# Kernel tuning notes

Hardware: AMD Instinct MI355X
Metric: run time of the kernel (lower is better)

Reference implementation:

```python
import jax, jax.numpy as jnp
import numpy as np

B, N, IN_DIM, EMB, HEADS, M, ITERS = 8, 4096, 1024, 512, 4, 256, 6
DH = EMB // HEADS
SCALE = DH ** -0.5
RES_K = 33  # residual depthwise conv kernel size (TransMIL / nystrom-attention default)


def setup_inputs() -> dict:
    key = jax.random.key(0)
    ks = iter(jax.random.split(key, 40))
    def rn(shape, s=0.02):
        return jax.random.normal(next(ks), shape, jnp.float32) * s
    inp = {"X": jax.random.normal(next(ks), (B, N, IN_DIM), jnp.float32)}
    inp["few_w"] = rn((IN_DIM, EMB)); inp["few_b"] = jnp.zeros((EMB,), jnp.float32)
    inp["cls_token"] = rn((1, 1, EMB), 1.0)
    for i in (1, 2):
        inp[f"l{i}_ln_g"] = jnp.ones((EMB,), jnp.float32)
        inp[f"l{i}_ln_b"] = jnp.zeros((EMB,), jnp.float32)
        inp[f"l{i}_qkv_w"] = rn((EMB, 3 * EMB))
        inp[f"l{i}_out_w"] = rn((EMB, EMB))
        inp[f"l{i}_out_b"] = jnp.zeros((EMB,), jnp.float32)
        inp[f"l{i}_res_k"] = rn((HEADS, 1, RES_K, 1))
    for ksz in (7, 5, 3):
        inp[f"ppeg_k{ksz}"] = rn((EMB, 1, ksz, ksz))
        inp[f"ppeg_b{ksz}"] = jnp.zeros((EMB,), jnp.float32)
    inp["norm_g"] = jnp.ones((EMB,), jnp.float32)
    inp["norm_b"] = jnp.zeros((EMB,), jnp.float32)
    inp["cls_w"] = rn((EMB, 1)); inp["cls_b"] = jnp.zeros((1,), jnp.float32)
    return inp


def _ln(x, g, b):
    mu = x.mean(-1, keepdims=True)
    var = x.var(-1, keepdims=True)
    return (x - mu) / jnp.sqrt(var + 1e-5) * g + b


def _pinv(x, iters):
    # Moore-Penrose iterative pseudo-inverse of (..., m, m)
    abs_x = jnp.abs(x)
    z = jnp.swapaxes(x, -1, -2) / (abs_x.sum(-1).max() * abs_x.sum(-2).max())
    I = jnp.eye(x.shape[-1], dtype=x.dtype)
    for _ in range(iters):
        xz = x @ z
        z = 0.25 * z @ (13 * I - xz @ (15 * I - xz @ (7 * I - xz)))
    return z


def _nystrom_layer(x, ln_g, ln_b, qkv_w, out_w, out_b, res_k):
    # pre-norm transformer layer with Nystrom attention + residual depthwise conv
    b, n, d = x.shape
    h = _ln(x, ln_g, ln_b)
    pad = (-n) % M  # left-pad so seq divisible by n_landmarks
    hp = jnp.pad(h, ((0, 0), (pad, 0), (0, 0)))
    n_p = n + pad
    q, k, v = jnp.split(hp @ qkv_w, 3, axis=-1)
    def to_heads(t):
        return t.reshape(b, n_p, HEADS, DH).transpose(0, 2, 1, 3)  # (b,h,n,dh)
    q, k, v = to_heads(q) * SCALE, to_heads(k), to_heads(v)
    l = n_p // M
    q_l = q.reshape(b, HEADS, M, l, DH).mean(3)  # landmark means
    k_l = k.reshape(b, HEADS, M, l, DH).mean(3)
    a1 = jax.nn.softmax(jnp.einsum('bhid,bhjd->bhij', q, k_l), -1)    # (b,h,n,m)
    a2 = jax.nn.softmax(jnp.einsum('bhid,bhjd->bhij', q_l, k_l), -1)  # (b,h,m,m)
    a3 = jax.nn.softmax(jnp.einsum('bhid,bhjd->bhij', q_l, k), -1)    # (b,h,m,n)
    out = a1 @ (_pinv(a2, ITERS) @ (a3 @ v))
    # residual depthwise conv over sequence, one channel per head
    res = jax.lax.conv_general_dilated(
        v, res_k, (1, 1), ((RES_K // 2, RES_K // 2), (0, 0)),
        dimension_numbers=('NCHW', 'OIHW', 'NCHW'), feature_group_count=HEADS)
    out = out + res
    out = out.transpose(0, 2, 1, 3).reshape(b, n_p, d) @ out_w + out_b
    return x + out[:, -n:]


def _dwconv(x, k, bias, pad):
    y = jax.lax.conv_general_dilated(
        x, k, (1, 1), ((pad, pad), (pad, pad)),
        dimension_numbers=('NCHW', 'OIHW', 'NCHW'), feature_group_count=EMB)
    return y + bias[None, :, None, None]


def _ppeg(x, H, W, k7, b7, k5, b5, k3, b3):
    b, _, c = x.shape
    cls_t, feat = x[:, :1], x[:, 1:]
    f = feat.transpose(0, 2, 1).reshape(b, c, H, W)
    y = f + _dwconv(f, k7, b7, 3) + _dwconv(f, k5, b5, 2) + _dwconv(f, k3, b3, 1)
    y = y.reshape(b, c, H * W).transpose(0, 2, 1)
    return jnp.concatenate([cls_t, y], axis=1)


def _forward(X, few_w, few_b, cls_token,
             l1_ln_g, l1_ln_b, l1_qkv_w, l1_out_w, l1_out_b, l1_res_k,
             l2_ln_g, l2_ln_b, l2_qkv_w, l2_out_w, l2_out_b, l2_res_k,
             ppeg_k7, ppeg_b7, ppeg_k5, ppeg_b5, ppeg_k3, ppeg_b3,
             norm_g, norm_b, cls_w, cls_b):
    b, bag = X.shape[0], X.shape[1]
    h = X @ few_w + few_b
    ps = int(np.ceil(np.sqrt(bag)))
    add = ps * ps - bag
    h = jnp.concatenate([h, h[:, :add]], axis=1)  # pad bag to perfect square
    h = jnp.concatenate([jnp.broadcast_to(cls_token, (b, 1, EMB)), h], axis=1)
    h = _nystrom_layer(h, l1_ln_g, l1_ln_b, l1_qkv_w, l1_out_w, l1_out_b, l1_res_k)
    h = _ppeg(h, ps, ps, ppeg_k7, ppeg_b7, ppeg_k5, ppeg_b5, ppeg_k3, ppeg_b3)
    h = _nystrom_layer(h, l2_ln_g, l2_ln_b, l2_qkv_w, l2_out_w, l2_out_b, l2_res_k)
    h = _ln(h, norm_g, norm_b)
    return (h[:, 0] @ cls_w + cls_b).squeeze(-1)  # (batch,) bag logits


def reference(X, few_w, few_b, cls_token,
              l1_ln_g, l1_ln_b, l1_qkv_w, l1_out_w, l1_out_b, l1_res_k,
              l2_ln_g, l2_ln_b, l2_qkv_w, l2_out_w, l2_out_b, l2_res_k,
              ppeg_k7, ppeg_b7, ppeg_k5, ppeg_b5, ppeg_k3, ppeg_b3,
              norm_g, norm_b, cls_w, cls_b):
    return _forward(X, few_w, few_b, cls_token,
                    l1_ln_g, l1_ln_b, l1_qkv_w, l1_out_w, l1_out_b, l1_res_k,
                    l2_ln_g, l2_ln_b, l2_qkv_w, l2_out_w, l2_out_b, l2_res_k,
                    ppeg_k7, ppeg_b7, ppeg_k5, ppeg_b5, ppeg_k3, ppeg_b3,
                    norm_g, norm_b, cls_w, cls_b)
```

## Files before the change

### kernel.cpp

```cpp
#include <hip/hip_runtime.h>

constexpr int BATCH = 8;
constexpr int NTOK  = 4097;
constexpr int NP    = 4352;
constexpr int PADR  = 255;
constexpr int EMBD  = 512;
constexpr int DHD   = 128;
constexpr int LSUB  = 17;
constexpr float SCALE_F = 0.08838834764831845f;

constexpr int PPS   = 72;
constexpr int PPLN  = 72 * 70;
constexpr long long TPAD_FLOATS = (long long)BATCH * EMBD * PPLN;

typedef unsigned short u16;
typedef short   s16x8 __attribute__((ext_vector_type(8)));
typedef u16     u16x4 __attribute__((ext_vector_type(4)));
typedef float   f32x4 __attribute__((ext_vector_type(4)));

__device__ __forceinline__ u16 f2bf(float x) {
    unsigned u = __float_as_uint(x);
    u += 0x7fffu + ((u >> 16) & 1u);
    return (u16)(u >> 16);
}
__device__ __forceinline__ float bf2f(u16 h) {
    return __uint_as_float(((unsigned)h) << 16);
}

__device__ __forceinline__ float block_sum256(float v) {
    __shared__ float tmp[4];
    __syncthreads();
#pragma unroll
    for (int off = 32; off > 0; off >>= 1) v += __shfl_down(v, off, 64);
    int t = threadIdx.x;
    if ((t & 63) == 0) tmp[t >> 6] = v;
    __syncthreads();
    return tmp[0] + tmp[1] + tmp[2] + tmp[3];
}

__device__ __forceinline__ float block_max256(float v) {
    __shared__ float tmp[4];
    __syncthreads();
#pragma unroll
    for (int off = 32; off > 0; off >>= 1) v = fmaxf(v, __shfl_down(v, off, 64));
    int t = threadIdx.x;
    if ((t & 63) == 0) tmp[t >> 6] = v;
    __syncthreads();
    return fmaxf(fmaxf(tmp[0], tmp[1]), fmaxf(tmp[2], tmp[3]));
}

struct GemmP {
    const float* A; const float* B; float* C; const float* bias;
    long long As1, As2, Bs1, Bs2, Cs1, Cs2;
    int Adiv, Bdiv, Cdiv;
    int Am, Bk, Bn, Cm, Arow, Crow;
    int M, N, K, nb;
    float alpha; int accum;
    float bdiagc; int btrans; float cdiagc; int ctrans;
};

constexpr int LDSTR = 40;
constexpr int AH = 0, AL = 2560, BHs = 5120, BLs = 7680;

__global__ __launch_bounds__(256) void gemm_k(GemmP p) {
    __shared__ u16 lds[10240];
    const int bz = blockIdx.z;
    const float* Ab = p.A + (long long)(bz / p.Adiv) * p.As1 + (long long)(bz % p.Adiv) * p.As2;
    const float* Bb = p.B + (long long)(bz / p.Bdiv) * p.Bs1 + (long long)(bz % p.Bdiv) * p.Bs2;
    float*       Cb = p.C + (long long)(bz / p.Cdiv) * p.Cs1 + (long long)(bz % p.Cdiv) * p.Cs2;
    const int m0 = blockIdx.y * 64, n0 = blockIdx.x * 64;
    const int t = threadIdx.x;
    const int wave = t >> 6, lane = t & 63;
    const int wm = (wave & 1) * 32, wn = (wave >> 1) * 32;
    const int quad = lane >> 4, l15 = lane & 15;

    f32x4 acc[2][2];
#pragma unroll
    for (int i = 0; i < 2; ++i)
#pragma unroll
        for (int j = 0; j < 2; ++j) acc[i][j] = (f32x4){0.f, 0.f, 0.f, 0.f};

    for (int k0 = 0; k0 < p.K; k0 += 32) {
        {
            const int ar = t >> 2, ac = (t & 3) * 8;
            float v[8];
            if (m0 + ar < p.M) {
                const float* s = Ab + (long long)(m0 + ar + p.Arow) * p.Am + (k0 + ac);
                float4 x0 = *(const float4*)s, x1 = *(const float4*)(s + 4);
                v[0] = x0.x; v[1] = x0.y; v[2] = x0.z; v[3] = x0.w;
                v[4] = x1.x; v[5] = x1.y; v[6] = x1.z; v[7] = x1.w;
            } else {
#pragma unroll
                for (int i = 0; i < 8; ++i) v[i] = 0.f;
            }
            u16 h[8], l[8];
#pragma unroll
            for (int i = 0; i < 8; ++i) { h[i] = f2bf(v[i]); l[i] = f2bf(v[i] - bf2f(h[i])); }
            const int off = ar * LDSTR + ac;
            u16x4 a0, a1, b0, b1;
#pragma unroll
            for (int i = 0; i < 4; ++i) { a0[i] = h[i]; a1[i] = h[i + 4]; b0[i] = l[i]; b1[i] = l[i + 4]; }
            *(u16x4*)&lds[AH + off] = a0; *(u16x4*)&lds[AH + off + 4] = a1;
            *(u16x4*)&lds[AL + off] = b0; *(u16x4*)&lds[AL + off + 4] = b1;
        }
        if (p.Bn == 1) {
            const int bk = t >> 3, n8 = (t & 7) * 8;
            const float* s = Bb + (long long)(k0 + bk) * p.Bk + (n0 + n8);
            float4 x0 = *(const float4*)s, x1 = *(const float4*)(s + 4);
            float v[8] = {x0.x, x0.y, x0.z, x0.w, x1.x, x1.y, x1.z, x1.w};
            if (p.btrans) {
                const int gk = k0 + bk;
#pragma unroll
                for (int i = 0; i < 8; ++i)
                    v[i] = (gk == n0 + n8 + i ? p.bdiagc : 0.f) - v[i];
            }
#pragma unroll
            for (int i = 0; i < 8; ++i) {
                int j = (i + (t & 7)) & 7;
                u16 h = f2bf(v[j]);
                lds[BHs + (n8 + j) * LDSTR + bk] = h;
                lds[BLs + (n8 + j) * LDSTR + bk] = f2bf(v[j] - bf2f(h));
            }
        } else {
            const int bn = t >> 2, k8 = (t & 3) * 8;
            const float* s = Bb + (long long)(n0 + bn) * p.Bn + (k0 + k8);
            float4 x0 = *(const float4*)s, x1 = *(const float4*)(s + 4);
            float v[8] = {x0.x, x0.y, x0.z, x0.w, x1.x, x1.y, x1.z, x1.w};
            u16 h[8], l[8];
#pragma unroll
            for (int i = 0; i < 8; ++i) { h[i] = f2bf(v[i]); l[i] = f2bf(v[i] - bf2f(h[i])); }
            const int off = bn * LDSTR + k8;
            u16x4 a0, a1, b0, b1;
#pragma unroll
            for (int i = 0; i < 4; ++i) { a0[i] = h[i]; a1[i] = h[i + 4]; b0[i] = l[i]; b1[i] = l[i + 4]; }
            *(u16x4*)&lds[BHs + off] = a0; *(u16x4*)&lds[BHs + off + 4] = a1;
            *(u16x4*)&lds[BLs + off] = b0; *(u16x4*)&lds[BLs + off + 4] = b1;
        }
        __syncthreads();

        s16x8 ah[2], al[2], bh[2], bl[2];
#pragma unroll
        for (int mi = 0; mi < 2; ++mi) {
            const int off = (wm + mi * 16 + l15) * LDSTR + quad * 8;
            u16x4 q0 = *(const u16x4*)&lds[AH + off], q1 = *(const u16x4*)&lds[AH + off + 4];
            u16x4 r0 = *(const u16x4*)&lds[AL + off], r1 = *(const u16x4*)&lds[AL + off + 4];
            s16x8 fh, fl;
#pragma unroll
            for (int i = 0; i < 4; ++i) { fh[i] = q0[i]; fh[i + 4] = q1[i]; fl[i] = r0[i]; fl[i + 4] = r1[i]; }
            ah[mi] = fh; al[mi] = fl;
        }
#pragma unroll
        for (int ni = 0; ni < 2; ++ni) {
            const int off = (wn + ni * 16 + l15) * LDSTR + quad * 8;
            u16x4 q0 = *(const u16x4*)&lds[BHs + off], q1 = *(const u16x4*)&lds[BHs + off + 4];
            u16x4 r0 = *(const u16x4*)&lds[BLs + off], r1 = *(const u16x4*)&lds[BLs + off + 4];
            s16x8 fh, fl;
#pragma unroll
            for (int i = 0; i < 4; ++i) { fh[i] = q0[i]; fh[i + 4] = q1[i]; fl[i] = r0[i]; fl[i + 4] = r1[i]; }
            bh[ni] = fh; bl[ni] = fl;
        }
#pragma unroll
        for (int mi = 0; mi < 2; ++mi)
#pragma unroll
            for (int ni = 0; ni < 2; ++ni) {
                acc[mi][ni] = __builtin_amdgcn_mfma_f32_16x16x32_bf16(ah[mi], bh[ni], acc[mi][ni], 0, 0, 0);
                acc[mi][ni] = __builtin_amdgcn_mfma_f32_16x16x32_bf16(ah[mi], bl[ni], acc[mi][ni], 0, 0, 0);
                acc[mi][ni] = __builtin_amdgcn_mfma_f32_16x16x32_bf16(al[mi], bh[ni], acc[mi][ni], 0, 0, 0);
            }
        __syncthreads();
    }

#pragma unroll
    for (int mi = 0; mi < 2; ++mi)
#pragma unroll
        for (int ni = 0; ni < 2; ++ni) {
            const int n = n0 + wn + ni * 16 + l15;
#pragma unroll
            for (int r = 0; r < 4; ++r) {
                const int m = m0 + wm + mi * 16 + quad * 4 + r;
                if (m >= p.M) continue;
                float v = p.alpha * acc[mi][ni][r];
                if (p.bias) v += p.bias[n];
                if (p.ctrans) v = (m == n ? p.cdiagc : 0.f) - v;
                float* dst = Cb + (long long)(m + p.Crow) * p.Cm + n;
                if (p.accum) *dst += v; else *dst = v;
            }
        }
}

__global__ void cls_set_k(float* H0, const float* cls) {
    int t = blockIdx.x * 256 + threadIdx.x;
    int b = t >> 9, c = t & 511;
    H0[(long long)b * NTOK * EMBD + c] = cls[c];
}

__global__ __launch_bounds__(256) void ln_pad_k(const float* __restrict__ H0,
                                                float* __restrict__ out,
                                                const float* g, const float* bb) {
    int row = blockIdx.x, b = blockIdx.y, t = threadIdx.x;
    float* o = out + ((long long)b * NP + row) * EMBD;
    if (row < PADR) { o[t] = 0.f; o[t + 256] = 0.f; return; }
    const float* x = H0 + ((long long)b * NTOK + (row - PADR)) * EMBD;
    float v0 = x[t], v1 = x[t + 256];
    float mu = block_sum256(v0 + v1) * (1.f / EMBD);
    float d0 = v0 - mu, d1 = v1 - mu;
    float var = block_sum256(d0 * d0 + d1 * d1) * (1.f / EMBD);
    float rs = 1.f / sqrtf(var + 1e-5f);
    o[t]       = d0 * rs * g[t]       + bb[t];
    o[t + 256] = d1 * rs * g[t + 256] + bb[t + 256];
}

__global__ void landmark_k(const float* __restrict__ QKV, float* __restrict__ QL,
                           float* __restrict__ KL) {
    long long idx = (long long)blockIdx.x * 256 + threadIdx.x;
    int d = idx & 127; int i = (int)((idx >> 7) & 255); int bh = (int)(idx >> 15);
    int b = bh >> 2, h = bh & 3;
    const float* base = QKV + (long long)b * NP * 1536 + (long long)i * LSUB * 1536 + h * DHD + d;
    float sq = 0.f, sk = 0.f;
#pragma unroll
    for (int j = 0; j < LSUB; ++j) { sq += base[j * 1536]; sk += base[j * 1536 + EMBD]; }
    QL[idx] = sq * (1.f / LSUB);
    KL[idx] = sk * (1.f / LSUB);
}

__global__ __launch_bounds__(256) void softmax256_k(float* __restrict__ X) {
    long long row = (long long)blockIdx.x * 4 + (threadIdx.x >> 6);
    int lane = threadIdx.x & 63;
    float4* p = (float4*)(X + row * 256) + lane;
    float4 v = *p;
    float m = fmaxf(fmaxf(v.x, v.y), fmaxf(v.z, v.w));
#pragma unroll
    for (int off = 32; off > 0; off >>= 1) m = fmaxf(m, __shfl_xor(m, off, 64));
    float ex = __expf(v.x - m), ey = __expf(v.y - m), ez = __expf(v.z - m), ew = __expf(v.w - m);
    float s = ex + ey + ez + ew;
#pragma unroll
    for (int off = 32; off > 0; off >>= 1) s += __shfl_xor(s, off, 64);
    float inv = 1.f / s;
    *p = make_float4(ex * inv, ey * inv, ez * inv, ew * inv);
}

__global__ __launch_bounds__(256) void softmax_k(float* __restrict__ X, int L) {
    float4* p = (float4*)(X + (long long)blockIdx.x * L);
    int nv = L >> 2, t = threadIdx.x;
    float m = -1e30f;
    for (int i = t; i < nv; i += 256) {
        float4 v = p[i];
        m = fmaxf(m, fmaxf(fmaxf(v.x, v.y), fmaxf(v.z, v.w)));
    }
    m = block_max256(m);
    float s = 0.f;
    for (int i = t; i < nv; i += 256) {
        float4 v = p[i];
        v.x = __expf(v.x - m); v.y = __expf(v.y - m); v.z = __expf(v.z - m); v.w = __expf(v.w - m);
        p[i] = v;
        s += v.x + v.y + v.z + v.w;
    }
    s = block_sum256(s);
    float inv = 1.f / s;
    for (int i = t; i < nv; i += 256) {
        float4 v = p[i];
        p[i] = make_float4(v.x * inv, v.y * inv, v.z * inv, v.w * inv);
    }
}

__global__ __launch_bounds__(256) void pinv_absmax_k(const float* __restrict__ X, float* red) {
    int bh = blockIdx.x, t = threadIdx.x;
    const float* x = X + (long long)bh * 65536;
    float rs = 0.f, cs = 0.f;
    for (int j = 0; j < 256; ++j) { rs += fabsf(x[t * 256 + j]); cs += fabsf(x[j * 256 + t]); }
    float mr = block_max256(rs);
    float mc = block_max256(cs);
    if (t == 0) { red[bh] = mr; red[32 + bh] = mc; }
}

__global__ void pinv_scalar_k(const float* red, float* inv) {
    float mr = 0.f, mc = 0.f;
    for (int i = 0; i < 32; ++i) { mr = fmaxf(mr, red[i]); mc = fmaxf(mc, red[32 + i]); }
    inv[0] = 1.f / (mr * mc);
}

__global__ void pinv_tinit_k(const float* __restrict__ X, const float* __restrict__ inv,
                             float* __restrict__ Z) {
    long long idx = (long long)blockIdx.x * 256 + threadIdx.x;
    int j = (int)(idx & 255); int i = (int)((idx >> 8) & 255); long long bh = idx >> 16;
    Z[idx] = X[(bh << 16) + ((long long)j << 8) + i] * inv[0];
}

__global__ void resconv_k(const float* __restrict__ QKV, const float* __restrict__ rk,
                          float* __restrict__ ATT2) {
    long long idx = (long long)blockIdx.x * 256 + threadIdx.x;
    if (idx >= (long long)BATCH * NTOK * EMBD) return;
    int c = (int)(idx & 511); long long r = idx >> 9;
    int n = PADR + (int)(r % NTOK); int b = (int)(r / NTOK);
    int h = c >> 7, d = c & 127;
    const float* vb = QKV + (long long)b * NP * 1536 + 1024 + h * DHD + d;
    float acc = 0.f;
#pragma unroll
    for (int u = 0; u < 33; ++u) {
        int nn = n + u - 16;
        if (nn >= 0 && nn < NP) acc += vb[(long long)nn * 1536] * rk[h * 33 + u];
    }
    ATT2[((long long)b * NP + n) * EMBD + c] += acc;
}

__global__ void wsum_k(const float* __restrict__ k7, const float* __restrict__ k5,
                       const float* __restrict__ k3, const float* __restrict__ b7,
                       const float* __restrict__ b5, const float* __restrict__ b3,
                       float* __restrict__ W) {
    int idx = blockIdx.x * 256 + threadIdx.x;
    if (idx < 25088) {
        int c = idx / 49, i = idx - c * 49;
        int dy = i / 7, dx = i - dy * 7;
        float w = k7[idx];
        if (dy >= 1 && dy <= 5 && dx >= 1 && dx <= 5) w += k5[c * 25 + (dy - 1) * 5 + (dx - 1)];
        if (dy >= 2 && dy <= 4 && dx >= 2 && dx <= 4) w += k3[c * 9 + (dy - 2) * 3 + (dx - 2)];
        W[idx] = w;
    } else if (idx < 25600) {
        int c = idx - 25088;
        W[25088 + c] = b7[c] + b5[c] + b3[c];
    }
}

__global__ __launch_bounds__(256) void tin_k(const float* __restrict__ H0,
                                             float* __restrict__ Tpad) {
    __shared__ float lds[64][65];
    const int y = blockIdx.x, c0 = blockIdx.y * 64, b = blockIdx.z;
    const int t = threadIdx.x;
    const int pc = t & 63, pr4 = t >> 6;
    const float* src = H0 + ((long long)b * NTOK + 1 + y * 64) * EMBD + c0;
#pragma unroll
    for (int i = 0; i < 16; ++i) {
        int pr = pr4 + i * 4;
        lds[pr][pc] = src[(long long)pr * EMBD + pc];
    }
    __syncthreads();
    const int xw = t & 63, cw4 = t >> 6;
#pragma unroll
    for (int i = 0; i < 16; ++i) {
        int cw = cw4 + i * 4;
        Tpad[(long long)(b * 512 + c0 + cw) * PPLN + (3 + y) * PPS + 3 + xw] = lds[xw][cw];
    }
}

__global__ __launch_bounds__(256, 4) void conv7_k(const float* __restrict__ Tpad,
                                                  const float* __restrict__ Wall,
                                                  float* __restrict__ Tout) {
    const int bc = blockIdx.x;
    const int c = bc & 511;
    const int t = threadIdx.x;
    const int x = t & 63, band = t >> 6;
    const int y0 = band * 16;
    const float* in = Tpad + (long long)bc * PPLN + x;
    float* outp = Tout + (long long)bc * 4096 + x;

    float W[49];
#pragma unroll
    for (int i = 0; i < 49; ++i) W[i] = Wall[c * 49 + i];
    const float bias = Wall[25088 + c];

    float win[7][7];
#pragma unroll
    for (int j = 0; j < 6; ++j)
#pragma unroll
        for (int d = 0; d < 7; ++d)
            win[j][d] = in[(y0 + j) * PPS + d];

#pragma unroll
    for (int yy = 0; yy < 16; ++yy) {
        const int slot = (6 + yy) % 7;
#pragma unroll
        for (int d = 0; d < 7; ++d)
            win[slot][d] = in[(y0 + yy + 6) * PPS + d];
        float s = bias + win[(yy + 3) % 7][3];
#pragma unroll
        for (int dy = 0; dy < 7; ++dy) {
            const int r = (yy + dy) % 7;
#pragma unroll
            for (int dx = 0; dx < 7; ++dx)
                s += W[dy * 7 + dx] * win[r][dx];
        }
        outp[(y0 + yy) * 64] = s;
    }
}

__global__ __launch_bounds__(256) void tout_k(const float* __restrict__ Tout,
                                              float* __restrict__ H0) {
    __shared__ float lds[64][65];
    const int y = blockIdx.x, c0 = blockIdx.y * 64, b = blockIdx.z;
    const int t = threadIdx.x;
    const int xl = t & 63, cl4 = t >> 6;
#pragma unroll
    for (int i = 0; i < 16; ++i) {
        int cl = cl4 + i * 4;
        lds[xl][cl] = Tout[(long long)(b * 512 + c0 + cl) * 4096 + y * 64 + xl];
    }
    __syncthreads();
    const int pc = t & 63, pl4 = t >> 6;
    float* dst = H0 + ((long long)b * NTOK + 1 + y * 64) * EMBD + c0;
#pragma unroll
    for (int i = 0; i < 16; ++i) {
        int pl = pl4 + i * 4;
        dst[(long long)pl * EMBD + pc] = lds[pl][pc];
    }
}

__global__ __launch_bounds__(256) void head_k(const float* __restrict__ H0, const float* g,
                                              const float* bb, const float* cw, const float* cb,
                                              float* __restrict__ out) {
    int b = blockIdx.x, t = threadIdx.x;
    const float* x = H0 + (long long)b * NTOK * EMBD;
    float v0 = x[t], v1 = x[t + 256];
    float mu = block_sum256(v0 + v1) * (1.f / EMBD);
    float d0 = v0 - mu, d1 = v1 - mu;
    float var = block_sum256(d0 * d0 + d1 * d1) * (1.f / EMBD);
    float rs = 1.f / sqrtf(var + 1e-5f);
    float y0 = d0 * rs * g[t] + bb[t];
    float y1 = d1 * rs * g[t + 256] + bb[t + 256];
    float s = block_sum256(y0 * cw[t] + y1 * cw[t + 256]);
    if (t == 0) out[b] = s + cb[0];
}

extern "C" void kernel_launch(void* const* d_in, const int* in_sizes, int n_in,
                              void* d_out, int out_size, void* d_ws, size_t ws_size,
                              hipStream_t stream) {
    (void)in_sizes; (void)n_in; (void)out_size; (void)ws_size;
    const float* X        = (const float*)d_in[0];
    const float* few_w    = (const float*)d_in[1];
    const float* few_b    = (const float*)d_in[2];
    const float* cls_tok  = (const float*)d_in[3];
    const float* ln_g[2]  = {(const float*)d_in[4],  (const float*)d_in[10]};
    const float* ln_b[2]  = {(const float*)d_in[5],  (const float*)d_in[11]};
    const float* qkv_w[2] = {(const float*)d_in[6],  (const float*)d_in[12]};
    const float* out_w[2] = {(const float*)d_in[7],  (const float*)d_in[13]};
    const float* out_b[2] = {(const float*)d_in[8],  (const float*)d_in[14]};
    const float* res_k[2] = {(const float*)d_in[9],  (const float*)d_in[15]};
    const float* k7 = (const float*)d_in[16]; const float* b7 = (const float*)d_in[17];
    const float* k5 = (const float*)d_in[18]; const float* b5 = (const float*)d_in[19];
    const float* k3 = (const float*)d_in[20]; const float* b3 = (const float*)d_in[21];
    const float* norm_g = (const float*)d_in[22]; const float* norm_b = (const float*)d_in[23];
    const float* cls_w  = (const float*)d_in[24]; const float* cls_b  = (const float*)d_in[25];
    float* out = (float*)d_out;

    float* ws  = (float*)d_ws;
    float* H0  = ws;
    float* LNH = H0  + 16781312LL;
    float* QKV = LNH + 17825792LL;
    float* A3  = QKV + 53477376LL;
    float* QL  = A3  + 35651584LL;
    float* KL  = QL  + 1048576LL;
    float* A2  = KL  + 1048576LL;
    float* KV  = A2  + 2097152LL;
    float* ZKV = KV  + 1048576LL;
    float* RED = ZKV + 1048576LL;
    float* Zb0 = A3;
    float* Zb1 = A3 + 2097152LL;
    float* XZm = A3 + 4194304LL;
    float* Tpad = QKV;
    float* Tout = QKV + TPAD_FLOATS;
    float* WSUM = A3;

    auto gemmx = [&](const float* A, long long As1, long long As2, int Adiv, int Am, int Arow,
                     const float* Bm, long long Bs1, long long Bs2, int Bdiv, int Bk, int Bn,
                     float* C, long long Cs1, long long Cs2, int Cdiv, int Cm, int Crow,
                     int M, int N, int K, int nb, float alpha, int accum, const float* bias,
                     float bdiagc, int btrans, float cdiagc, int ctrans) {
        GemmP p;
        p.A = A; p.B = Bm; p.C = C; p.bias = bias;
        p.As1 = As1; p.As2 = As2; p.Bs1 = Bs1; p.Bs2 = Bs2; p.Cs1 = Cs1; p.Cs2 = Cs2;
        p.Adiv = Adiv; p.Bdiv = Bdiv; p.Cdiv = Cdiv;
        p.Am = Am; p.Bk = Bk; p.Bn = Bn; p.Cm = Cm; p.Arow = Arow; p.Crow = Crow;
        p.M = M; p.N = N; p.K = K; p.nb = nb; p.alpha = alpha; p.accum = accum;
        p.bdiagc = bdiagc; p.btrans = btrans; p.cdiagc = cdiagc; p.ctrans = ctrans;
        dim3 grid(N / 64, (M + 63) / 64, nb);
        gemm_k<<<grid, 256, 0, stream>>>(p);
    };
    auto gemm = [&](const float* A, long long As1, long long As2, int Adiv, int Am, int Arow,
                    const float* Bm, long long Bs1, long long Bs2, int Bdiv, int Bk, int Bn,
                    float* C, long long Cs1, long long Cs2, int Cdiv, int Cm, int Crow,
                    int M, int N, int K, int nb, float alpha, int accum, const float* bias) {
        gemmx(A, As1, As2, Adiv, Am, Arow, Bm, Bs1, Bs2, Bdiv, Bk, Bn,
              C, Cs1, Cs2, Cdiv, Cm, Crow, M, N, K, nb, alpha, accum, bias, 0.f, 0, 0.f, 0);
    };

    cls_set_k<<<16, 256, 0, stream>>>(H0, cls_tok);
    gemm(X, 4194304LL, 0, 1, 1024, 0,
         few_w, 0, 0, 1, 512, 1,
         H0, 2097664LL, 0, 1, 512, 1,
         4096, 512, 1024, BATCH, 1.f, 0, few_b);

    for (int L = 0; L < 2; ++L) {
        ln_pad_k<<<dim3(NP, BATCH), 256, 0, stream>>>(H0, LNH, ln_g[L], ln_b[L]);
        gemm(LNH, 0, 0, 1, 512, 0,
             qkv_w[L], 0, 0, 1, 1536, 1,
             QKV, 0, 0, 1, 1536, 0,
             BATCH * NP, 1536, 512, 1, 1.f, 0, nullptr);
        landmark_k<<<4096, 256, 0, stream>>>(QKV, QL, KL);
        gemm(QL, 32768LL, 0, 1, 128, 0,
             KL, 32768LL, 0, 1, 1, 128,
             A2, 65536LL, 0, 1, 256, 0,
             256, 256, 128, 32, SCALE_F, 0, nullptr);
        softmax256_k<<<2048, 256, 0, stream>>>(A2);
        gemm(QL, 32768LL, 0, 1, 128, 0,
             QKV + 512, 6680064LL, 128LL, 4, 1, 1536,
             A3, 1114112LL, 0, 1, 4352, 0,
             256, 4352, 128, 32, SCALE_F, 0, nullptr);
        softmax_k<<<8192, 256, 0, stream>>>(A3, 4352);
        gemm(A3, 1114112LL, 0, 1, 4352, 0,
             QKV + 1024, 6680064LL, 128LL, 4, 1536, 1,
             KV, 32768LL, 0, 1, 128, 0,
             256, 128, 4352, 32, 1.f, 0, nullptr);
        pinv_absmax_k<<<32, 256, 0, stream>>>(A2, RED);
        pinv_scalar_k<<<1, 1, 0, stream>>>(RED, RED + 64);
        pinv_tinit_k<<<8192, 256, 0, stream>>>(A2, RED + 64, Zb0);
        float* zc = Zb0; float* zn = Zb1;
        for (int it = 0; it < 6; ++it) {
            float* U1 = A3 + 6291456LL;
            float* U2 = A3 + 8388608LL;
            gemm(A2, 65536LL, 0, 1, 256, 0, zc, 65536LL, 0, 1, 256, 1,
                 XZm, 65536LL, 0, 1, 256, 0, 256, 256, 256, 32, 1.f, 0, nullptr);
            gemmx(XZm, 65536LL, 0, 1, 256, 0, XZm, 65536LL, 0, 1, 256, 1,
                  U1, 65536LL, 0, 1, 256, 0, 256, 256, 256, 32, 1.f, 0, nullptr,
                  7.f, 1, 15.f, 1);
            gemmx(XZm, 65536LL, 0, 1, 256, 0, U1, 65536LL, 0, 1, 256, 1,
                  U2, 65536LL, 0, 1, 256, 0, 256, 256, 256, 32, 1.f, 0, nullptr,
                  0.f, 0, 13.f, 1);
            gemm(zc, 65536LL, 0, 1, 256, 0, U2, 65536LL, 0, 1, 256, 1,
                 zn, 65536LL, 0, 1, 256, 0, 256, 256, 256, 32, 0.25f, 0, nullptr);
            float* t2 = zc; zc = zn; zn = t2;
        }
        gemm(zc, 65536LL, 0, 1, 256, 0,
             KV, 32768LL, 0, 1, 128, 1,
             ZKV, 32768LL, 0, 1, 128, 0,
             256, 128, 256, 32, 1.f, 0, nullptr);
        gemm(QKV, 6680064LL, 128LL, 4, 1536, 0,
             KL, 32768LL, 0, 1, 1, 128,
             A3, 1114112LL, 0, 1, 256, 0,
             4352, 256, 128, 32, SCALE_F, 0, nullptr);
        softmax256_k<<<34816, 256, 0, stream>>>(A3);
        gemm(A3, 1114112LL, 0, 1, 256, 0,
             ZKV, 32768LL, 0, 1, 128, 1,
             LNH, 2228224LL, 128LL, 4, 512, 0,
             4352, 128, 256, 32, 1.f, 0, nullptr);
        resconv_k<<<65552, 256, 0, stream>>>(QKV, res_k[L], LNH);
        gemm(LNH, 2228224LL, 0, 1, 512, PADR,
             out_w[L], 0, 0, 1, 512, 1,
             H0, 2097664LL, 0, 1, 512, 0,
             NTOK, 512, 512, BATCH, 1.f, 1, out_b[L]);

        if (L == 0) {
            hipMemsetAsync(Tpad, 0, TPAD_FLOATS * sizeof(float), stream);
            wsum_k<<<101, 256, 0, stream>>>(k7, k5, k3, b7, b5, b3, WSUM);
            tin_k<<<dim3(64, 8, 8), 256, 0, stream>>>(H0, Tpad);
            conv7_k<<<4096, 256, 0, stream>>>(Tpad, WSUM, Tout);
            tout_k<<<dim3(64, 8, 8), 256, 0, stream>>>(Tout, H0);
        }
    }

    head_k<<<BATCH, 256, 0, stream>>>(H0, norm_g, norm_b, cls_w, cls_b, out);
}
```

Measured before the change: 4.561 ms.

## Add split-bf16 3-pass MFMA GEMM for large projections and attention scores

Adds a new GEMM kernel using a larger 128x256 tile that multiplies split bf16 hi/lo pairs with three MFMA passes (hi*hi, hi*lo, lo*hi) to approximate fp32 accuracy. It is used for the feature, QKV and output projections and for the two big landmark score GEMMs. Operands are pre-split by new split/transpose kernels, and LayerNorm now writes hi/lo bf16 directly. The kernel-3 softmax GEMM is moved earlier and workspace buffers are re-aliased. The extra split passes and memory traffic are the cost, and the three-pass bf16 scheme may lose a little accuracy.

```diff
diff --git a/kernel.cpp b/kernel.cpp
--- a/kernel.cpp
+++ b/kernel.cpp
@@ -188,6 +188,141 @@
         }
 }
 
+struct SplitP {
+    const float* src; u16* dh; u16* dl;
+    long long s1, s2, rstride, dstride, total;
+    int div, R, C8;
+    float scale;
+};
+__global__ __launch_bounds__(256) void split_k(SplitP p) {
+    long long idx = (long long)blockIdx.x * 256 + threadIdx.x;
+    if (idx >= p.total) return;
+    int c8 = (int)(idx % p.C8);
+    long long tmp = idx / p.C8;
+    int r  = (int)(tmp % p.R);
+    int bz = (int)(tmp / p.R);
+    const float* s = p.src + (long long)(bz / p.div) * p.s1 + (long long)(bz % p.div) * p.s2
+                   + (long long)r * p.rstride + c8 * 8;
+    float4 x0 = *(const float4*)s, x1 = *(const float4*)(s + 4);
+    float v[8] = {x0.x, x0.y, x0.z, x0.w, x1.x, x1.y, x1.z, x1.w};
+    s16x8 hv, lv;
+#pragma unroll
+    for (int i = 0; i < 8; ++i) {
+        float sv = v[i] * p.scale;
+        u16 h = f2bf(sv);
+        hv[i] = (short)h;
+        lv[i] = (short)f2bf(sv - bf2f(h));
+    }
+    long long doff = (long long)bz * p.dstride + (long long)r * (p.C8 * 8) + c8 * 8;
+    *(s16x8*)&p.dh[doff] = hv;
+    *(s16x8*)&p.dl[doff] = lv;
+}
+
+__global__ __launch_bounds__(256) void splitT_k(const float* __restrict__ src,
+                                                u16* __restrict__ dh, u16* __restrict__ dl,
+                                                int K, int N) {
+    int idx = blockIdx.x * 256 + threadIdx.x;
+    if (idx >= N * K) return;
+    int n = idx / K, k = idx - n * K;
+    float v = src[(long long)k * N + n];
+    u16 h = f2bf(v);
+    dh[idx] = h;
+    dl[idx] = f2bf(v - bf2f(h));
+}
+
+struct GemmBtP {
+    const u16 *Ah, *Al, *Bh, *Bl;
+    float* C; const float* bias;
+    long long Abs, Bbs, Cbs;
+    int M, N, K, Cm, Crow, accum;
+};
+
+__global__ __launch_bounds__(256, 2) void gemm_bt_k(GemmBtP p) {
+    __shared__ u16 lds[10240];
+    const int bz = blockIdx.z;
+    const u16* Ahb = p.Ah + (long long)bz * p.Abs;
+    const u16* Alb = p.Al + (long long)bz * p.Abs;
+    const u16* Bhb = p.Bh + (long long)bz * p.Bbs;
+    const u16* Blb = p.Bl + (long long)bz * p.Bbs;
+    float*     Cb  = p.C  + (long long)bz * p.Cbs;
+    const int m0 = blockIdx.y * 128, n0 = blockIdx.x * 256;
+    const int t = threadIdx.x;
+    const int wave = t >> 6, lane = t & 63;
+    const int wm = (wave & 1) * 64, wn = (wave >> 1) * 128;
+    const int quad = lane >> 4, l15 = lane & 15;
+    const int K = p.K;
+
+    const int r0 = t >> 2, c0 = (t & 3) * 8;
+    const int ga0 = (m0 + r0      < p.M) ? (m0 + r0)      : (p.M - 1);
+    const int ga1 = (m0 + r0 + 64 < p.M) ? (m0 + r0 + 64) : (p.M - 1);
+    const long long arow0 = (long long)ga0 * K + c0;
+    const long long arow1 = (long long)ga1 * K + c0;
+    const long long bb0   = (long long)(n0 + wn + l15) * K + quad * 8;
+    const long long bstep = 16LL * K;
+    const int wof = r0 * LDSTR + c0;
+
+    f32x4 acc[4][8];
+#pragma unroll
+    for (int i = 0; i < 4; ++i)
+#pragma unroll
+        for (int j = 0; j < 8; ++j) acc[i][j] = (f32x4){0.f, 0.f, 0.f, 0.f};
+
+    s16x8 sa0, sa1, sl0, sl1;
+    auto LOADA = [&](int k0) {
+        sa0 = *(const s16x8*)&Ahb[arow0 + k0];
+        sa1 = *(const s16x8*)&Ahb[arow1 + k0];
+        sl0 = *(const s16x8*)&Alb[arow0 + k0];
+        sl1 = *(const s16x8*)&Alb[arow1 + k0];
+    };
+    LOADA(0);
+
+    for (int k0 = 0; k0 < K; k0 += 32) {
+        *(s16x8*)&lds[wof]               = sa0;
+        *(s16x8*)&lds[wof + 2560]        = sa1;
+        *(s16x8*)&lds[5120 + wof]        = sl0;
+        *(s16x8*)&lds[5120 + wof + 2560] = sl1;
+        __syncthreads();
+        if (k0 + 32 < K) LOADA(k0 + 32);
+
+        s16x8 bh[8], bl[8];
+#pragma unroll
+        for (int ni = 0; ni < 8; ++ni) {
+            const long long bo = bb0 + ni * bstep + k0;
+            bh[ni] = *(const s16x8*)&Bhb[bo];
+            bl[ni] = *(const s16x8*)&Blb[bo];
+        }
+#pragma unroll
+        for (int mi = 0; mi < 4; ++mi) {
+            const int off = (wm + mi * 16 + l15) * LDSTR + quad * 8;
+            s16x8 ah = *(const s16x8*)&lds[off];
+            s16x8 al = *(const s16x8*)&lds[5120 + off];
+#pragma unroll
+            for (int ni = 0; ni < 8; ++ni) {
+                acc[mi][ni] = __builtin_amdgcn_mfma_f32_16x16x32_bf16(ah, bh[ni], acc[mi][ni], 0, 0, 0);
+                acc[mi][ni] = __builtin_amdgcn_mfma_f32_16x16x32_bf16(ah, bl[ni], acc[mi][ni], 0, 0, 0);
+                acc[mi][ni] = __builtin_amdgcn_mfma_f32_16x16x32_bf16(al, bh[ni], acc[mi][ni], 0, 0, 0);
+            }
+        }
+        __syncthreads();
+    }
+
+#pragma unroll
+    for (int mi = 0; mi < 4; ++mi)
+#pragma unroll
+        for (int ni = 0; ni < 8; ++ni) {
+            const int n = n0 + wn + ni * 16 + l15;
+            const float bv = p.bias ? p.bias[n] : 0.f;
+#pragma unroll
+            for (int r = 0; r < 4; ++r) {
+                const int m = m0 + wm + mi * 16 + quad * 4 + r;
+                if (m >= p.M) continue;
+                float* dst = Cb + (long long)(m + p.Crow) * p.Cm + n;
+                float v = acc[mi][ni][r] + bv;
+                if (p.accum) *dst += v; else *dst = v;
+            }
+        }
+}
+
 __global__ void cls_set_k(float* H0, const float* cls) {
     int t = blockIdx.x * 256 + threadIdx.x;
     int b = t >> 9, c = t & 511;
@@ -195,19 +330,25 @@
 }
 
 __global__ __launch_bounds__(256) void ln_pad_k(const float* __restrict__ H0,
-                                                float* __restrict__ out,
+                                                u16* __restrict__ oh, u16* __restrict__ ol,
                                                 const float* g, const float* bb) {
     int row = blockIdx.x, b = blockIdx.y, t = threadIdx.x;
-    float* o = out + ((long long)b * NP + row) * EMBD;
-    if (row < PADR) { o[t] = 0.f; o[t + 256] = 0.f; return; }
+    long long off = ((long long)b * NP + row) * EMBD;
+    if (row < PADR) {
+        oh[off + t] = 0; oh[off + t + 256] = 0;
+        ol[off + t] = 0; ol[off + t + 256] = 0;
+        return;
+    }
     const float* x = H0 + ((long long)b * NTOK + (row - PADR)) * EMBD;
     float v0 = x[t], v1 = x[t + 256];
     float mu = block_sum256(v0 + v1) * (1.f / EMBD);
     float d0 = v0 - mu, d1 = v1 - mu;
     float var = block_sum256(d0 * d0 + d1 * d1) * (1.f / EMBD);
     float rs = 1.f / sqrtf(var + 1e-5f);
-    o[t]       = d0 * rs * g[t]       + bb[t];
-    o[t + 256] = d1 * rs * g[t + 256] + bb[t + 256];
+    float y0 = d0 * rs * g[t]       + bb[t];
+    float y1 = d1 * rs * g[t + 256] + bb[t + 256];
+    u16 h0 = f2bf(y0); oh[off + t]       = h0; ol[off + t]       = f2bf(y0 - bf2f(h0));
+    u16 h1 = f2bf(y1); oh[off + t + 256] = h1; ol[off + t + 256] = f2bf(y1 - bf2f(h1));
 }
 
 __global__ void landmark_k(const float* __restrict__ QKV, float* __restrict__ QL,
@@ -452,9 +593,26 @@
     float* KV  = A2  + 2097152LL;
     float* ZKV = KV  + 1048576LL;
     float* RED = ZKV + 1048576LL;
-    float* Zb0 = A3;
-    float* Zb1 = A3 + 2097152LL;
-    float* XZm = A3 + 4194304LL;
+
+    u16* LNHh = (u16*)LNH;
+    u16* LNHl = (u16*)(LNH + 8912896LL);
+    u16* QLh  = (u16*)KV;
+    u16* QLl  = (u16*)(KV + 524288LL);
+    u16* KLh  = (u16*)ZKV;
+    u16* KLl  = (u16*)(ZKV + 524288LL);
+    u16* Xh   = (u16*)A3;
+    u16* Xl   = (u16*)(A3 + 16777216LL);
+    u16* ATh  = (u16*)A3;
+    u16* ATl  = (u16*)(A3 + 8390656LL);
+    u16* Wh   = (u16*)A2;
+    u16* fwl  = (u16*)(A2 + 262144LL);
+    u16* qwl  = (u16*)(A2 + 393216LL);
+    u16* owl  = (u16*)(A2 + 131072LL);
+    float* Zb0 = LNH;
+    float* Zb1 = LNH + 2097152LL;
+    float* XZm = LNH + 4194304LL;
+    float* U1  = LNH + 6291456LL;
+    float* U2  = LNH + 8388608LL;
     float* Tpad = QKV;
     float* Tout = QKV + TPAD_FLOATS;
     float* WSUM = A3;
@@ -481,41 +639,71 @@
         gemmx(A, As1, As2, Adiv, Am, Arow, Bm, Bs1, Bs2, Bdiv, Bk, Bn,
               C, Cs1, Cs2, Cdiv, Cm, Crow, M, N, K, nb, alpha, accum, bias, 0.f, 0, 0.f, 0);
     };
+    auto split = [&](const float* src, u16* dh, u16* dl, long long s1, long long s2, int div,
+                     long long rstride, int R, int C, int nb, float scale) {
+        SplitP p;
+        p.src = src; p.dh = dh; p.dl = dl;
+        p.s1 = s1; p.s2 = s2; p.div = div;
+        p.rstride = rstride; p.R = R; p.C8 = C >> 3;
+        p.dstride = (long long)R * C;
+        p.total = (long long)nb * R * (C >> 3);
+        p.scale = scale;
+        int blocks = (int)((p.total + 255) / 256);
+        split_k<<<blocks, 256, 0, stream>>>(p);
+    };
+    auto gemmbt = [&](const u16* Ah, const u16* Al, long long Abs,
+                      const u16* Bh, const u16* Bl, long long Bbs,
+                      float* C, long long Cbs, int Cm, int Crow,
+                      int M, int N, int K, int nb, int accum, const float* bias) {
+        GemmBtP p;
+        p.Ah = Ah; p.Al = Al; p.Bh = Bh; p.Bl = Bl;
+        p.C = C; p.bias = bias;
+        p.Abs = Abs; p.Bbs = Bbs; p.Cbs = Cbs;
+        p.M = M; p.N = N; p.K = K; p.Cm = Cm; p.Crow = Crow; p.accum = accum;
+        dim3 grid(N / 256, (M + 127) / 128, nb);
+        gemm_bt_k<<<grid, 256, 0, stream>>>(p);
+    };
 
     cls_set_k<<<16, 256, 0, stream>>>(H0, cls_tok);
-    gemm(X, 4194304LL, 0, 1, 1024, 0,
-         few_w, 0, 0, 1, 512, 1,
-         H0, 2097664LL, 0, 1, 512, 1,
-         4096, 512, 1024, BATCH, 1.f, 0, few_b);
+    split(X, Xh, Xl, 0, 0, 1, 1024, 32768, 1024, 1, 1.f);
+    splitT_k<<<2048, 256, 0, stream>>>(few_w, Wh, fwl, 1024, 512);
+    gemmbt(Xh, Xl, 4194304LL, Wh, fwl, 0,
+           H0, 2097664LL, 512, 1,
+           4096, 512, 1024, BATCH, 0, few_b);
 
     for (int L = 0; L < 2; ++L) {
-        ln_pad_k<<<dim3(NP, BATCH), 256, 0, stream>>>(H0, LNH, ln_g[L], ln_b[L]);
-        gemm(LNH, 0, 0, 1, 512, 0,
-             qkv_w[L], 0, 0, 1, 1536, 1,
-             QKV, 0, 0, 1, 1536, 0,
-             BATCH * NP, 1536, 512, 1, 1.f, 0, nullptr);
+        ln_pad_k<<<dim3(NP, BATCH), 256, 0, stream>>>(H0, LNHh, LNHl, ln_g[L], ln_b[L]);
+        splitT_k<<<3072, 256, 0, stream>>>(qkv_w[L], Wh, qwl, 512, 1536);
+        gemmbt(LNHh, LNHl, 0, Wh, qwl, 0,
+               QKV, 0, 1536, 0,
+               34816, 1536, 512, 1, 0, nullptr);
         landmark_k<<<4096, 256, 0, stream>>>(QKV, QL, KL);
         gemm(QL, 32768LL, 0, 1, 128, 0,
              KL, 32768LL, 0, 1, 1, 128,
              A2, 65536LL, 0, 1, 256, 0,
              256, 256, 128, 32, SCALE_F, 0, nullptr);
         softmax256_k<<<2048, 256, 0, stream>>>(A2);
-        gemm(QL, 32768LL, 0, 1, 128, 0,
-             QKV + 512, 6680064LL, 128LL, 4, 1, 1536,
-             A3, 1114112LL, 0, 1, 4352, 0,
-             256, 4352, 128, 32, SCALE_F, 0, nullptr);
+        split(QL, QLh, QLl, 32768LL, 0, 1, 128, 256, 128, 32, SCALE_F);
+        split(KL, KLh, KLl, 32768LL, 0, 1, 128, 256, 128, 32, 1.f);
+        split(QKV + 512, LNHh, LNHl, 6680064LL, 128LL, 4, 1536, 4352, 128, 32, 1.f);
+        gemmbt(QLh, QLl, 32768LL, LNHh, LNHl, 557056LL,
+               A3, 1114112LL, 4352, 0,
+               256, 4352, 128, 32, 0, nullptr);
         softmax_k<<<8192, 256, 0, stream>>>(A3, 4352);
         gemm(A3, 1114112LL, 0, 1, 4352, 0,
              QKV + 1024, 6680064LL, 128LL, 4, 1536, 1,
              KV, 32768LL, 0, 1, 128, 0,
              256, 128, 4352, 32, 1.f, 0, nullptr);
+        split(QKV, LNHh, LNHl, 6680064LL, 128LL, 4, 1536, 4352, 128, 32, SCALE_F);
+        gemmbt(LNHh, LNHl, 557056LL, KLh, KLl, 32768LL,
+               A3, 1114112LL, 256, 0,
+               4352, 256, 128, 32, 0, nullptr);
+        softmax256_k<<<34816, 256, 0, stream>>>(A3);
         pinv_absmax_k<<<32, 256, 0, stream>>>(A2, RED);
         pinv_scalar_k<<<1, 1, 0, stream>>>(RED, RED + 64);
         pinv_tinit_k<<<8192, 256, 0, stream>>>(A2, RED + 64, Zb0);
         float* zc = Zb0; float* zn = Zb1;
         for (int it = 0; it < 6; ++it) {
-            float* U1 = A3 + 6291456LL;
-            float* U2 = A3 + 8388608LL;
             gemm(A2, 65536LL, 0, 1, 256, 0, zc, 65536LL, 0, 1, 256, 1,
                  XZm, 65536LL, 0, 1, 256, 0, 256, 256, 256, 32, 1.f, 0, nullptr);
             gemmx(XZm, 65536LL, 0, 1, 256, 0, XZm, 65536LL, 0, 1, 256, 1,
@@ -532,20 +720,16 @@
              KV, 32768LL, 0, 1, 128, 1,
              ZKV, 32768LL, 0, 1, 128, 0,
              256, 128, 256, 32, 1.f, 0, nullptr);
-        gemm(QKV, 6680064LL, 128LL, 4, 1536, 0,
-             KL, 32768LL, 0, 1, 1, 128,
-             A3, 1114112LL, 0, 1, 256, 0,
-             4352, 256, 128, 32, SCALE_F, 0, nullptr);
-        softmax256_k<<<34816, 256, 0, stream>>>(A3);
         gemm(A3, 1114112LL, 0, 1, 256, 0,
              ZKV, 32768LL, 0, 1, 128, 1,
              LNH, 2228224LL, 128LL, 4, 512, 0,
              4352, 128, 256, 32, 1.f, 0, nullptr);
         resconv_k<<<65552, 256, 0, stream>>>(QKV, res_k[L], LNH);
-        gemm(LNH, 2228224LL, 0, 1, 512, PADR,
-             out_w[L], 0, 0, 1, 512, 1,
-             H0, 2097664LL, 0, 1, 512, 0,
-             NTOK, 512, 512, BATCH, 1.f, 1, out_b[L]);
+        split(LNH + PADR * 512, ATh, ATl, 2228224LL, 0, 1, 512, 4097, 512, 8, 1.f);
+        splitT_k<<<1024, 256, 0, stream>>>(out_w[L], Wh, owl, 512, 512);
+        gemmbt(ATh, ATl, 2097664LL, Wh, owl, 0,
+               H0, 2097664LL, 512, 0,
+               4097, 512, 512, BATCH, 1, out_b[L]);
 
         if (L == 0) {
             hipMemsetAsync(Tpad, 0, TPAD_FLOATS * sizeof(float), stream);
```

After: 4.626 ms. Within noise of the previous version (+1.4%).
